# Kernel tuning notes

Hardware: AMD Instinct MI355X
Metric: run time of the kernel (lower is better)

The kernel has to match this reference:

```python
import jax, jax.numpy as jnp
import numpy as np

B = 16           # number of graphs
H = 8            # heads
NC = 9           # num_coeffs = (lmax+1)^2
DM = 128         # d_model (sphere_channels)
F = NC * DM      # flat_dim = 1152
HD = F // H      # head_dim = 144
RD = 16          # rope_dim
EPS = 1e-5


def setup_inputs() -> dict:
    key = jax.random.key(0)
    ks = jax.random.split(key, 8)
    N = 8192
    x_emb = jax.random.normal(ks[0], (N, NC, DM), dtype=jnp.float32)
    batch = jnp.sort(jax.random.randint(ks[1], (N,), 0, B)).astype(jnp.int32)
    pos = jax.random.normal(ks[2], (N, 3), dtype=jnp.float32) * 3.0
    Wqkv = jax.random.normal(ks[3], (F, 3 * F), dtype=jnp.float32) / np.sqrt(F)
    Wout = jax.random.normal(ks[4], (F, F), dtype=jnp.float32) / np.sqrt(F)
    rope_freqs = jax.random.normal(ks[5], (RD,), dtype=jnp.float32) * 0.1
    Wrope = jax.random.normal(ks[6], (RD, H), dtype=jnp.float32) / np.sqrt(RD)
    gamma = jnp.ones((F,), dtype=jnp.float32)
    beta = jnp.zeros((F,), dtype=jnp.float32)
    return {"x_emb": x_emb, "pos": pos, "Wqkv": Wqkv, "Wout": Wout,
            "rope_freqs": rope_freqs, "Wrope": Wrope,
            "gamma": gamma, "beta": beta, "batch": batch}


def _pad_layout(batch, N):
    # sorted batch ids -> per-node rank within its graph, sizes per graph
    sizes = jnp.bincount(batch, length=B)                       # [B]
    offsets = jnp.concatenate([jnp.zeros((1,), sizes.dtype), jnp.cumsum(sizes)[:-1]])
    rank = jnp.arange(N, dtype=sizes.dtype) - offsets[batch]    # [N]
    n_max = int(np.asarray(jax.device_get(sizes)).max())        # concrete pad width
    return sizes, rank, n_max


def reference(x_emb, pos, Wqkv, Wout, rope_freqs, Wrope, gamma, beta, batch):
    N = x_emb.shape[0]
    x_flat = x_emb.reshape(N, F)
    sizes, rank, n_max = _pad_layout(batch, N)

    # dense padding  [B, N_max, *]; mask True = padding slot
    x_pad = jnp.zeros((B, n_max, F), x_flat.dtype).at[batch, rank].set(x_flat)
    pos_pad = jnp.zeros((B, n_max, 3), pos.dtype).at[batch, rank].set(pos)
    mask = jnp.arange(n_max)[None, :] >= sizes[:, None]         # [B, N_max]

    qkv = x_pad @ Wqkv                                          # [B, N_max, 3F]
    q, k, v = jnp.split(qkv, 3, axis=-1)
    def heads(t):
        return t.reshape(B, n_max, H, HD).transpose(0, 2, 1, 3)  # [B,H,N_max,HD]
    q, k, v = heads(q), heads(k), heads(v)

    scale = HD ** (-0.5)
    attn = jnp.einsum('bhid,bhjd->bhij', q, k) * scale          # [B,H,N,N]

    # Fourier distance bias
    diff = pos_pad[:, :, None, :] - pos_pad[:, None, :, :]      # [B,N,N,3]
    dist = jnp.linalg.norm(diff, axis=-1)                       # [B,N,N]
    fourier = jnp.cos(dist[..., None] * jnp.abs(rope_freqs))    # [B,N,N,RD]
    bias = jnp.einsum('bijr,rh->bhij', fourier, Wrope)          # [B,H,N,N]
    pad_mask = mask[:, None, :] | mask[:, :, None]              # [B,N,N]
    bias = jnp.where(pad_mask[:, None, :, :], 0.0, bias)
    attn = attn + bias

    attn = jnp.where(mask[:, None, None, :], -jnp.inf, attn)    # key mask
    attn = jax.nn.softmax(attn, axis=-1)
    attn = jnp.nan_to_num(attn)

    out = jnp.einsum('bhij,bhjd->bhid', attn, v)                # [B,H,N,HD]
    out = out.transpose(0, 2, 1, 3).reshape(B, n_max, F) @ Wout
    out_flat = out[batch, rank]                                 # gather back [N,F]

    h = x_flat + out_flat
    mu = jnp.mean(h, axis=-1, keepdims=True)
    var = jnp.var(h, axis=-1, keepdims=True)
    y = (h - mu) / jnp.sqrt(var + EPS) * gamma + beta
    return y.reshape(N, NC, DM)
```

## Files before the change

kernel.cpp:

```cpp
#include <hip/hip_runtime.h>

typedef unsigned short u16;
typedef unsigned int   u32;
typedef __attribute__((ext_vector_type(8)))  __bf16 bf16x8;
typedef __attribute__((ext_vector_type(4)))  float  f32x4;
typedef __attribute__((ext_vector_type(16))) float  f32x16;
typedef __attribute__((ext_vector_type(4)))  u32    u32x4;
typedef __attribute__((ext_vector_type(2)))  u32    u32x2;

#define F_DIM   1152
#define QKV_DIM 3456
#define HD_SCALE 0.083333333333333333f
#define LOG2E    1.4426950408889634f
#define KSC      (HD_SCALE*LOG2E)
#define MAX4    80
#define BIAS_BLKS 2048

static __device__ __forceinline__ u16 f2bf(float f){
    u32 u = __builtin_bit_cast(u32, f);
    u32 r = u + 0x7fffu + ((u >> 16) & 1u);
    return (u16)(r >> 16);
}
static __device__ __forceinline__ u32 cvtpk(float lo, float hi){
    u32 r;
    asm("v_cvt_pk_bf16_f32 %0, %1, %2" : "=v"(r) : "v"(lo), "v"(hi));
    return r;
}

typedef __attribute__((address_space(1))) void gvoid;
typedef __attribute__((address_space(3))) void lvoid;
static __device__ __forceinline__ void gload16(const u16* g, u16* l){
    __builtin_amdgcn_global_load_lds((gvoid*)g, (lvoid*)l, 16, 0, 0);
}

__global__ __launch_bounds__(256) void prep_kernel(
        const float* __restrict__ x, u16* __restrict__ xb, int nCast, int n4,
        const float* __restrict__ Wqkv, u16* __restrict__ wqkvT,
        const float* __restrict__ Wout, u16* __restrict__ woutT,
        const float* __restrict__ pos, const float* __restrict__ rfreq,
        const float* __restrict__ Wrope, u16* __restrict__ biasP,
        const int* __restrict__ batch, int* __restrict__ meta, int N){
    __shared__ float tile[32][33];
    __shared__ int goffs[17];
    __shared__ int bpre[17];
    const int b = blockIdx.x, t = threadIdx.x;
    const int T1 = (QKV_DIM/32)*(F_DIM/32);
    const int T2 = (F_DIM/32)*(F_DIM/32);

    if (b < BIAS_BLKS){
        if (t <= 16){
            int lo = 0, hi = N;
            while (lo < hi){ int mid = (lo+hi)>>1; if (batch[mid] < t) lo = mid+1; else hi = mid; }
            goffs[t] = lo;
        }
        __syncthreads();
        if (t == 0){
            int bc = 0;
            for (int g = 0; g < 16; g++){
                bpre[g] = bc;
                int ng = goffs[g+1] - goffs[g];
                int ntg = (ng + 31) >> 5;
                bc += ntg*ntg;
            }
            bpre[16] = bc;
        }
        __syncthreads();
        float absf[16], w[16][8];
        #pragma unroll
        for (int r = 0; r < 16; r++){
            absf[r] = fabsf(rfreq[r]);
            #pragma unroll
            for (int h = 0; h < 8; h++) w[r][h] = Wrope[r*8 + h] * LOG2E;
        }
        const int total = bpre[16];
        for (int bb = b; bb < total; bb += BIAS_BLKS){
            int g = 0;
            while (bpre[g+1] <= bb) g++;
            int rem  = bb - bpre[g];
            int goff = goffs[g];
            int ng   = goffs[g+1] - goff;
            int ntg  = (ng + 31) >> 5;
            int qt   = rem / ntg;
            int jt   = rem - qt*ntg;
            size_t base = (size_t)bb * 8192;
            #pragma unroll
            for (int pp = 0; pp < 2; pp++){
                const int p0 = pp*512 + 2*t;
                float bv0[8], bv1[8];
                #pragma unroll
                for (int h = 0; h < 8; h++){ bv0[h] = 0.f; bv1[h] = 0.f; }
                const int i = p0 >> 5;
                int qn = goff + qt*32 + i;  if (qn >= goff + ng) qn = goff + ng - 1;
                float qx = pos[qn*3+0], qy = pos[qn*3+1], qz = pos[qn*3+2];
                #pragma unroll
                for (int e = 0; e < 2; e++){
                    int c = (p0 + e) & 31;
                    int p4 = c & 15;
                    int j  = (p4 & 3) + ((p4 >> 2) << 3) + ((c >> 4) << 2);
                    int kn = goff + jt*32 + j;  if (kn >= goff + ng) kn = goff + ng - 1;
                    float dx = qx - pos[kn*3+0];
                    float dy = qy - pos[kn*3+1];
                    float dz = qz - pos[kn*3+2];
                    float d  = sqrtf(dx*dx + dy*dy + dz*dz);
                    float* bv = e ? bv1 : bv0;
                    #pragma unroll
                    for (int r = 0; r < 16; r++){
                        float cs = __cosf(d * absf[r]);
                        #pragma unroll
                        for (int h = 0; h < 8; h++) bv[h] = fmaf(cs, w[r][h], bv[h]);
                    }
                }
                #pragma unroll
                for (int h = 0; h < 8; h++)
                    *(u32*)&biasP[base + h*1024 + p0] = cvtpk(bv0[h], bv1[h]);
            }
        }
        return;
    }
    const int b2 = b - BIAS_BLKS;
    if (b2 < nCast){
        int i = b2*256 + t;
        if (i < n4){
            float4 v = ((const float4*)x)[i];
            u32x2 o; o[0] = cvtpk(v.x, v.y); o[1] = cvtpk(v.z, v.w);
            *(u32x2*)&xb[(size_t)i*4] = o;
        }
        return;
    }
    if (b2 < nCast + T1 + T2){
        const float* in; u16* out; int R, C, bi;
        if (b2 < nCast + T1){ in = Wqkv; out = wqkvT; R = F_DIM; C = QKV_DIM; bi = b2 - nCast; }
        else                { in = Wout; out = woutT; R = F_DIM; C = F_DIM;  bi = b2 - nCast - T1; }
        int gx = C/32;
        int c0 = (bi % gx)*32, r0 = (bi / gx)*32;
        int tx = t & 31, ty = t >> 5;
        #pragma unroll
        for (int yy = ty; yy < 32; yy += 8)
            tile[yy][tx] = in[(size_t)(r0+yy)*C + (c0+tx)];
        __syncthreads();
        #pragma unroll
        for (int yy = ty; yy < 32; yy += 8)
            out[(size_t)(c0+yy)*R + (r0+tx)] = f2bf(tile[tx][yy]);
        return;
    }
    if (t <= 16){
        int lo = 0, hi = N;
        while (lo < hi){ int mid = (lo+hi)>>1; if (batch[mid] < t) lo = mid+1; else hi = mid; }
        meta[1+t] = lo;
    }
    __syncthreads();
    if (t == 0){
        int ps = 0, bcnt = 0, cnt4 = 0;
        for (int g = 0; g < 16; g++){
            int ng = meta[2+g] - meta[1+g];
            meta[20+g] = ps;
            meta[40+g] = bcnt;
            int nt = (ng + 31) / 32;
            ps += nt * 32;
            bcnt += nt * nt;
            int nt4 = (nt + 3) / 4;
            for (int q4 = 0; q4 < nt4; q4++){
                meta[64 + cnt4] = g;
                meta[64 + MAX4 + cnt4] = q4;
                cnt4++;
            }
        }
        meta[36] = ps;
        meta[56] = bcnt;
        meta[0]  = cnt4;
    }
}

template<bool OUT_BF16>
__global__ __launch_bounds__(512, 2) void gemm256(const u16* __restrict__ A,
                                                  const u16* __restrict__ Bt,
                                                  void* __restrict__ Cp,
                                                  int M, int Ncols, int K){
    __shared__ u16 sA[4][8192];
    __shared__ u16 sB[4][8192];
    const int nwg = gridDim.x;
    int orig = blockIdx.x;
    int qq = nwg >> 3, rr = nwg & 7;
    int xcd = orig & 7, pos = orig >> 3;
    int nid = (xcd < rr ? xcd*(qq+1) : rr*(qq+1) + (xcd-rr)*qq) + pos;
    const int gx = M >> 8;
    const int bm = (nid % gx) << 8, bn = (nid / gx) << 8;

    const int tid = threadIdx.x;
    const int w = tid >> 6, lane = tid & 63;
    const int wr = w >> 2, wc = w & 3;
    const int fr = lane & 15, fq = lane >> 4;
    const int swz8 = (fq ^ ((fr >> 1) & 3)) * 8;

    const u16* aS[2]; const u16* bS[2]; int dOf[2];
    #pragma unroll
    for (int p = 0; p < 2; p++){
        int idx = p*512 + tid;
        int row = idx >> 2, c = idx & 3;
        int sc = c ^ ((row >> 1) & 3);
        int brow = bn + row; if (brow > Ncols-1) brow = Ncols-1;
        aS[p] = A  + (size_t)(bm + row)*K + sc*8;
        bS[p] = Bt + (size_t)brow*K + sc*8;
        dOf[p] = idx*8;
    }

    f32x4 acc[8][4];
    #pragma unroll
    for (int m = 0; m < 8; m++)
        #pragma unroll
        for (int n = 0; n < 4; n++)
            #pragma unroll
            for (int e = 0; e < 4; e++) acc[m][n][e] = 0.f;

    const int nk = K >> 5;
    #pragma unroll
    for (int p = 0; p < 2; p++){ gload16(aS[p], &sA[0][dOf[p]]); gload16(bS[p], &sB[0][dOf[p]]); }
    #pragma unroll
    for (int p = 0; p < 2; p++){ gload16(aS[p]+32, &sA[1][dOf[p]]); gload16(bS[p]+32, &sB[1][dOf[p]]); }

    #pragma unroll 1
    for (int t = 0; t < nk; t++){
        int tp = (t+2 < nk) ? t+2 : nk-1;
        int bufS = (t+2) & 3;
        #pragma unroll
        for (int p = 0; p < 2; p++){
            gload16(aS[p] + tp*32, &sA[bufS][dOf[p]]);
            gload16(bS[p] + tp*32, &sB[bufS][dOf[p]]);
        }
        asm volatile("s_waitcnt vmcnt(8)\n\ts_barrier" ::: "memory");

        const u16* sAc = &sA[t & 3][0];
        const u16* sBc = &sB[t & 3][0];
        bf16x8 af[8], bfr[4];
        #pragma unroll
        for (int m = 0; m < 8; m++)
            af[m] = *(const bf16x8*)(sAc + (wr*128 + m*16 + fr)*32 + swz8);
        #pragma unroll
        for (int n = 0; n < 4; n++)
            bfr[n] = *(const bf16x8*)(sBc + (wc*64 + n*16 + fr)*32 + swz8);
        __builtin_amdgcn_s_setprio(1);
        #pragma unroll
        for (int m = 0; m < 8; m++)
            #pragma unroll
            for (int n = 0; n < 4; n++)
                acc[m][n] = __builtin_amdgcn_mfma_f32_16x16x32_bf16(af[m], bfr[n], acc[m][n], 0, 0, 0);
        __builtin_amdgcn_s_setprio(0);
    }

    #pragma unroll
    for (int m = 0; m < 8; m++)
        #pragma unroll
        for (int n = 0; n < 4; n++)
            #pragma unroll
            for (int r = 0; r < 4; r++){
                int row = bm + wr*128 + m*16 + fq*4 + r;
                int col = bn + wc*64 + n*16 + fr;
                if (col < Ncols){
                    float v = acc[m][n][r];
                    if (OUT_BF16) ((u16*)Cp)[(size_t)row*Ncols + col] = f2bf(v);
                    else          ((float*)Cp)[(size_t)row*Ncols + col] = v;
                }
            }
}

__global__ __launch_bounds__(256) void pack_v(const u16* __restrict__ qkv,
                                              u16* __restrict__ Vpack,
                                              const int* __restrict__ batch,
                                              const int* __restrict__ meta,
                                              int PT){
    __shared__ u16 tile[32][33];
    int nt0 = blockIdx.x*32, dt0 = blockIdx.y*32, h = blockIdx.z;
    int tx = threadIdx.x & 31, ty = threadIdx.x >> 5;
    #pragma unroll
    for (int yy = ty; yy < 32; yy += 8){
        int node = nt0+yy, d = dt0+tx;
        tile[yy][tx] = (d < 144) ? qkv[(size_t)node*QKV_DIM + 2*F_DIM + h*144 + d] : (u16)0;
    }
    __syncthreads();
    int node = nt0 + tx;
    int g = batch[node];
    int col = meta[20+g] + (node - meta[1+g]);
    int pt = col >> 5, cl = col & 31;
    #pragma unroll
    for (int yy = ty; yy < 32; yy += 8){
        int d = dt0+yy;
        if (d < 144) Vpack[(((size_t)h*PT + pt)*144 + d)*32 + cl] = tile[tx][yy];
    }
}

__global__ __launch_bounds__(256) void attn_kernel(
        const u16* __restrict__ qkv, const u16* __restrict__ Vpack,
        const u16* __restrict__ biasP, u16* __restrict__ attn_out,
        const int* __restrict__ meta, int PT){
    __shared__ u16 sK[2][4864];
    __shared__ u16 sV[2][4608];
    const int h = blockIdx.x & 7, t4 = blockIdx.x >> 3;
    if (t4 >= meta[0]) return;
    const int g    = meta[64 + t4];
    const int q4   = meta[64 + MAX4 + t4];
    const int goff = meta[1+g], gend = meta[2+g];
    const int ng   = gend - goff;
    const int ntg  = (ng + 31) >> 5;
    const int pst  = meta[20+g];
    const int boffg= meta[40+g];

    const int tid = threadIdx.x;
    const int w = tid >> 6, lane = tid & 63;
    const int li = lane & 31, hi = lane >> 5;
    const int qt = q4*4 + w;
    const int qbase = goff + qt*32;
    const int qtP = (qt < ntg) ? qt : (ntg - 1);

    int kOff[3];
    #pragma unroll
    for (int p = 0; p < 3; p++){
        int idx = p*256 + tid;
        if (idx > 607) idx = 607;
        int row = idx/19, c = idx - row*19;
        if (c == 18) c = 0;
        kOff[p] = row*QKV_DIM + c*8;
    }
    const u16* kBase = qkv + (size_t)goff*QKV_DIM + F_DIM + h*144;
    int vOff[3];
    #pragma unroll
    for (int p = 0; p < 3; p++){
        int idx = p*256 + tid;
        if (idx > 575) idx = 575;
        int d = idx >> 2, c = idx & 3;
        vOff[p] = d*32 + ((c ^ (d & 3)) << 3);
    }
    const u16* vBase = Vpack + ((size_t)h*PT + (pst >> 5))*4608;
    const u16* bBase = biasP + ((size_t)boffg + (size_t)qtP*ntg)*8192 + h*1024 + li*32 + hi*16;

    int qnode = qbase + li; if (qnode >= gend) qnode = gend - 1;
    const u16* qrow = qkv + (size_t)qnode*QKV_DIM + h*144;
    bf16x8 qf[9];
    #pragma unroll
    for (int kk = 0; kk < 9; kk++) qf[kk] = *(const bf16x8*)(qrow + kk*16 + hi*8);

    int jlr[16];
    #pragma unroll
    for (int r = 0; r < 16; r++) jlr[r] = (r & 3) + ((r >> 2) << 3) + (hi << 2);

    float lrun = 0.f;
    f32x16 O[5];
    #pragma unroll
    for (int dt = 0; dt < 5; dt++)
        #pragma unroll
        for (int e = 0; e < 16; e++) O[dt][e] = 0.f;

    u32x4 bA0, bA1, bN0, bN1;
    bA0 = *(const u32x4*)bBase;
    bA1 = *(const u32x4*)(bBase + 8);
    {
        gload16(kBase + kOff[0], &sK[0][tid*8]);
        gload16(kBase + kOff[1], &sK[0][(256+tid)*8]);
        if (tid < 96) gload16(kBase + kOff[2], &sK[0][(512+tid)*8]);
        gload16(vBase + vOff[0], &sV[0][tid*8]);
        gload16(vBase + vOff[1], &sV[0][(256+tid)*8]);
        if (tid < 64) gload16(vBase + vOff[2], &sV[0][(512+tid)*8]);
    }
    __syncthreads();

    #pragma unroll 1
    for (int t = 0; t < ntg; t++){
        const int cur = t & 1;
        int tn = (t+1 < ntg) ? t+1 : ntg-1;
        bN0 = *(const u32x4*)(bBase + (size_t)tn*8192);
        bN1 = *(const u32x4*)(bBase + (size_t)tn*8192 + 8);
        __builtin_amdgcn_sched_barrier(0);
        if (t+1 < ntg){
            const u16* kb = kBase + (size_t)(t+1)*32*QKV_DIM;
            const u16* vb = vBase + (size_t)(t+1)*4608;
            gload16(kb + kOff[0], &sK[cur^1][tid*8]);
            gload16(kb + kOff[1], &sK[cur^1][(256+tid)*8]);
            if (tid < 96) gload16(kb + kOff[2], &sK[cur^1][(512+tid)*8]);
            gload16(vb + vOff[0], &sV[cur^1][tid*8]);
            gload16(vb + vOff[1], &sV[cur^1][(256+tid)*8]);
            if (tid < 64) gload16(vb + vOff[2], &sV[cur^1][(512+tid)*8]);
        }

        const u16* sKc = &sK[cur][0];
        f32x16 sacc;
        #pragma unroll
        for (int e = 0; e < 16; e++) sacc[e] = 0.f;
        __builtin_amdgcn_s_setprio(1);
        #pragma unroll
        for (int kk = 0; kk < 9; kk++){
            bf16x8 kf = *(const bf16x8*)(sKc + li*152 + kk*16 + hi*8);
            sacc = __builtin_amdgcn_mfma_f32_32x32x16_bf16(kf, qf[kk], sacc, 0, 0, 0);
        }
        __builtin_amdgcn_s_setprio(0);

        float bfv[16];
        #pragma unroll
        for (int q = 0; q < 4; q++){
            bfv[2*q]     = __builtin_bit_cast(float, bA0[q] << 16);
            bfv[2*q+1]   = __builtin_bit_cast(float, bA0[q] & 0xffff0000u);
            bfv[8+2*q]   = __builtin_bit_cast(float, bA1[q] << 16);
            bfv[8+2*q+1] = __builtin_bit_cast(float, bA1[q] & 0xffff0000u);
        }

        const int j0 = t*32;
        float p[16];
        float psum = 0.f;
        if (j0 + 32 <= ng){
            #pragma unroll
            for (int r = 0; r < 16; r++){
                float s_ = fminf(fmaf(sacc[r], KSC, bfv[r]), 86.f);
                p[r] = exp2f(s_); psum += p[r];
            }
        } else {
            #pragma unroll
            for (int r = 0; r < 16; r++){
                float s_ = fminf(fmaf(sacc[r], KSC, bfv[r]), 86.f);
                p[r] = (j0 + jlr[r] < ng) ? exp2f(s_) : 0.f;
                psum += p[r];
            }
        }
        psum += __shfl_xor(psum, 32);
        lrun += psum;

        u32 cpk[8], opk[8];
        #pragma unroll
        for (int q = 0; q < 8; q++) cpk[q] = cvtpk(p[2*q], p[2*q+1]);
        #pragma unroll
        for (int q = 0; q < 8; q++) opk[q] = (u32)__shfl_xor((int)cpk[q], 32);
        u32x4 a0, a1;
        if (hi == 0){
            a0[0]=cpk[0]; a0[1]=cpk[1]; a0[2]=opk[0]; a0[3]=opk[1];
            a1[0]=cpk[4]; a1[1]=cpk[5]; a1[2]=opk[4]; a1[3]=opk[5];
        } else {
            a0[0]=opk[2]; a0[1]=opk[3]; a0[2]=cpk[2]; a0[3]=cpk[3];
            a1[0]=opk[6]; a1[1]=opk[7]; a1[2]=cpk[6]; a1[3]=cpk[7];
        }
        bf16x8 paf0 = __builtin_bit_cast(bf16x8, a0);
        bf16x8 paf1 = __builtin_bit_cast(bf16x8, a1);

        const u16* sVc = &sV[cur][0];
        __builtin_amdgcn_s_setprio(1);
        #pragma unroll
        for (int dt = 0; dt < 5; dt++){
            int d = dt*32 + li;
            int dc = (d > 143) ? 143 : d;
            int swzlo = ((hi     ^ (dc & 3)) << 3);
            int swzhi = (((2+hi) ^ (dc & 3)) << 3);
            bf16x8 v0 = *(const bf16x8*)(sVc + dc*32 + swzlo);
            bf16x8 v1 = *(const bf16x8*)(sVc + dc*32 + swzhi);
            O[dt] = __builtin_amdgcn_mfma_f32_32x32x16_bf16(paf0, v0, O[dt], 0, 0, 0);
            O[dt] = __builtin_amdgcn_mfma_f32_32x32x16_bf16(paf1, v1, O[dt], 0, 0, 0);
        }
        __builtin_amdgcn_s_setprio(0);

        bA0 = bN0; bA1 = bN1;
        __syncthreads();
    }

    if (qt < ntg){
        float lr[16];
        #pragma unroll
        for (int r = 0; r < 16; r++) lr[r] = 1.0f / __shfl(lrun, jlr[r]);
        #pragma unroll
        for (int dt = 0; dt < 5; dt++){
            int d = dt*32 + li;
            if (d < 144){
                #pragma unroll
                for (int r = 0; r < 16; r++){
                    int qi = jlr[r];
                    if (qt*32 + qi < ng)
                        attn_out[(size_t)(qbase + qi)*F_DIM + h*144 + d] = f2bf(O[dt][r]*lr[r]);
                }
            }
        }
    }
}

__global__ __launch_bounds__(256) void ln_kernel(const float* __restrict__ x,
                                                 float* __restrict__ io,
                                                 const float* __restrict__ gamma,
                                                 const float* __restrict__ beta){
    const int node = blockIdx.x;
    const float* xr = x  + (size_t)node*F_DIM;
    float* yr       = io + (size_t)node*F_DIM;
    const int t = threadIdx.x;
    float h[5]; float s = 0.f, ss = 0.f;
    #pragma unroll
    for (int i = 0; i < 5; i++){
        int idx = t + i*256;
        float v = 0.f;
        if (idx < F_DIM) v = xr[idx] + yr[idx];
        h[i] = v; s += v; ss += v*v;
    }
    #pragma unroll
    for (int o = 32; o > 0; o >>= 1){ s += __shfl_down(s, o); ss += __shfl_down(ss, o); }
    __shared__ float rs[4], rss[4];
    __shared__ float smu, srstd;
    if ((t & 63) == 0){ rs[t>>6] = s; rss[t>>6] = ss; }
    __syncthreads();
    if (t == 0){
        float S  = rs[0]+rs[1]+rs[2]+rs[3];
        float SS = rss[0]+rss[1]+rss[2]+rss[3];
        float mu = S * (1.f/F_DIM);
        float var = SS * (1.f/F_DIM) - mu*mu;
        smu = mu; srstd = rsqrtf(var + 1e-5f);
    }
    __syncthreads();
    float mu = smu, rstd = srstd;
    #pragma unroll
    for (int i = 0; i < 5; i++){
        int idx = t + i*256;
        if (idx < F_DIM) yr[idx] = (h[i]-mu)*rstd*gamma[idx] + beta[idx];
    }
}

extern "C" void kernel_launch(void* const* d_in, const int* in_sizes, int n_in,
                              void* d_out, int out_size, void* d_ws, size_t ws_size,
                              hipStream_t stream){
    const float* x     = (const float*)d_in[0];
    const float* pos   = (const float*)d_in[1];
    const float* Wqkv  = (const float*)d_in[2];
    const float* Wout  = (const float*)d_in[3];
    const float* rfreq = (const float*)d_in[4];
    const float* Wrope = (const float*)d_in[5];
    const float* gamma = (const float*)d_in[6];
    const float* beta  = (const float*)d_in[7];
    const int*   batch = (const int*)d_in[8];

    const int N  = in_sizes[0] / F_DIM;
    const int PN = N + 512;
    const int PT = PN / 32;

    char* ws = (char*)d_ws;
    size_t off = 0;
    auto alloc = [&](size_t b){ size_t o = off; off += (b + 255) & ~(size_t)255; return o; };
    int* meta   = (int*)(ws + alloc((size_t)(64 + 2*MAX4 + 64)*sizeof(int)));
    u16* xb     = (u16*)(ws + alloc((size_t)N*F_DIM*2));
    u16* wqkvT  = (u16*)(ws + alloc((size_t)QKV_DIM*F_DIM*2));
    u16* woutT  = (u16*)(ws + alloc((size_t)F_DIM*F_DIM*2));
    u16* qkv    = (u16*)(ws + alloc((size_t)N*QKV_DIM*2));
    u16* Vpack  = (u16*)(ws + alloc((size_t)8*PT*144*32*2));
    u16* biasb  = (u16*)(ws + off);
    (void)ws_size; (void)n_in; (void)out_size;

    const int n4    = N*F_DIM/4;
    const int nCast = (n4 + 255)/256;
    const int nT    = (QKV_DIM/32)*(F_DIM/32) + (F_DIM/32)*(F_DIM/32);
    hipLaunchKernelGGL(prep_kernel, dim3(BIAS_BLKS + nCast + nT + 1), dim3(256), 0, stream,
                       x, xb, nCast, n4, Wqkv, wqkvT, Wout, woutT,
                       pos, rfreq, Wrope, biasb, batch, meta, N);
    hipLaunchKernelGGL((gemm256<true>), dim3((N/256)*((QKV_DIM+255)/256)), dim3(512), 0, stream,
                       xb, wqkvT, (void*)qkv, N, QKV_DIM, F_DIM);
    hipLaunchKernelGGL(pack_v, dim3(N/32, 5, 8), dim3(256), 0, stream,
                       qkv, Vpack, batch, meta, PT);
    hipLaunchKernelGGL(attn_kernel, dim3(MAX4*8), dim3(256), 0, stream,
                       qkv, Vpack, biasb, xb, meta, PT);
    hipLaunchKernelGGL((gemm256<false>), dim3((N/256)*((F_DIM+255)/256)), dim3(512), 0, stream,
                       xb, woutT, d_out, N, F_DIM, F_DIM);
    hipLaunchKernelGGL(ln_kernel, dim3(N), dim3(256), 0, stream,
                       x, (float*)d_out, gamma, beta);
}
```

Measured before the change: 287.3 us.

## Interleave bias compute and memory-bound prep work within persistent prep blocks

```diff
diff --git a/kernel.cpp b/kernel.cpp
--- a/kernel.cpp
+++ b/kernel.cpp
@@ -14,7 +14,7 @@
 #define LOG2E    1.4426950408889634f
 #define KSC      (HD_SCALE*LOG2E)
 #define MAX4    80
-#define BIAS_BLKS 2048
+#define PREP_BLKS 4096
 
 static __device__ __forceinline__ u16 f2bf(float f){
     u32 u = __builtin_bit_cast(u32, f);
@@ -46,25 +46,27 @@
     const int b = blockIdx.x, t = threadIdx.x;
     const int T1 = (QKV_DIM/32)*(F_DIM/32);
     const int T2 = (F_DIM/32)*(F_DIM/32);
-
-    if (b < BIAS_BLKS){
-        if (t <= 16){
-            int lo = 0, hi = N;
-            while (lo < hi){ int mid = (lo+hi)>>1; if (batch[mid] < t) lo = mid+1; else hi = mid; }
-            goffs[t] = lo;
-        }
-        __syncthreads();
-        if (t == 0){
-            int bc = 0;
-            for (int g = 0; g < 16; g++){
-                bpre[g] = bc;
-                int ng = goffs[g+1] - goffs[g];
-                int ntg = (ng + 31) >> 5;
-                bc += ntg*ntg;
-            }
-            bpre[16] = bc;
-        }
-        __syncthreads();
+    const int NMEM = nCast + T1 + T2 + 1;
+
+    if (t <= 16){
+        int lo = 0, hi = N;
+        while (lo < hi){ int mid = (lo+hi)>>1; if (batch[mid] < t) lo = mid+1; else hi = mid; }
+        goffs[t] = lo;
+    }
+    __syncthreads();
+    if (t == 0){
+        int bc = 0;
+        for (int g = 0; g < 16; g++){
+            bpre[g] = bc;
+            int ng = goffs[g+1] - goffs[g];
+            int ntg = (ng + 31) >> 5;
+            bc += ntg*ntg;
+        }
+        bpre[16] = bc;
+    }
+    __syncthreads();
+
+    auto do_bias = [&](){
         float absf[16], w[16][8];
         #pragma unroll
         for (int r = 0; r < 16; r++){
@@ -73,7 +75,7 @@
             for (int h = 0; h < 8; h++) w[r][h] = Wrope[r*8 + h] * LOG2E;
         }
         const int total = bpre[16];
-        for (int bb = b; bb < total; bb += BIAS_BLKS){
+        for (int bb = b; bb < total; bb += PREP_BLKS){
             int g = 0;
             while (bpre[g+1] <= bb) g++;
             int rem  = bb - bpre[g];
@@ -115,60 +117,61 @@
                     *(u32*)&biasP[base + h*1024 + p0] = cvtpk(bv0[h], bv1[h]);
             }
         }
-        return;
-    }
-    const int b2 = b - BIAS_BLKS;
-    if (b2 < nCast){
-        int i = b2*256 + t;
-        if (i < n4){
-            float4 v = ((const float4*)x)[i];
-            u32x2 o; o[0] = cvtpk(v.x, v.y); o[1] = cvtpk(v.z, v.w);
-            *(u32x2*)&xb[(size_t)i*4] = o;
-        }
-        return;
-    }
-    if (b2 < nCast + T1 + T2){
-        const float* in; u16* out; int R, C, bi;
-        if (b2 < nCast + T1){ in = Wqkv; out = wqkvT; R = F_DIM; C = QKV_DIM; bi = b2 - nCast; }
-        else                { in = Wout; out = woutT; R = F_DIM; C = F_DIM;  bi = b2 - nCast - T1; }
-        int gx = C/32;
-        int c0 = (bi % gx)*32, r0 = (bi / gx)*32;
-        int tx = t & 31, ty = t >> 5;
-        #pragma unroll
-        for (int yy = ty; yy < 32; yy += 8)
-            tile[yy][tx] = in[(size_t)(r0+yy)*C + (c0+tx)];
-        __syncthreads();
-        #pragma unroll
-        for (int yy = ty; yy < 32; yy += 8)
-            out[(size_t)(c0+yy)*R + (r0+tx)] = f2bf(tile[tx][yy]);
-        return;
-    }
-    if (t <= 16){
-        int lo = 0, hi = N;
-        while (lo < hi){ int mid = (lo+hi)>>1; if (batch[mid] < t) lo = mid+1; else hi = mid; }
-        meta[1+t] = lo;
-    }
-    __syncthreads();
-    if (t == 0){
-        int ps = 0, bcnt = 0, cnt4 = 0;
-        for (int g = 0; g < 16; g++){
-            int ng = meta[2+g] - meta[1+g];
-            meta[20+g] = ps;
-            meta[40+g] = bcnt;
-            int nt = (ng + 31) / 32;
-            ps += nt * 32;
-            bcnt += nt * nt;
-            int nt4 = (nt + 3) / 4;
-            for (int q4 = 0; q4 < nt4; q4++){
-                meta[64 + cnt4] = g;
-                meta[64 + MAX4 + cnt4] = q4;
-                cnt4++;
+    };
+
+    auto do_mem = [&](){
+        for (int u = b; u < NMEM; u += PREP_BLKS){
+            if (u < nCast){
+                int i = u*256 + t;
+                if (i < n4){
+                    float4 v = ((const float4*)x)[i];
+                    u32x2 o; o[0] = cvtpk(v.x, v.y); o[1] = cvtpk(v.z, v.w);
+                    *(u32x2*)&xb[(size_t)i*4] = o;
+                }
+            } else if (u < nCast + T1 + T2){
+                const float* in; u16* out; int R, C, bi;
+                if (u < nCast + T1){ in = Wqkv; out = wqkvT; R = F_DIM; C = QKV_DIM; bi = u - nCast; }
+                else               { in = Wout; out = woutT; R = F_DIM; C = F_DIM;  bi = u - nCast - T1; }
+                int gx = C/32;
+                int c0 = (bi % gx)*32, r0 = (bi / gx)*32;
+                int tx = t & 31, ty = t >> 5;
+                __syncthreads();
+                #pragma unroll
+                for (int yy = ty; yy < 32; yy += 8)
+                    tile[yy][tx] = in[(size_t)(r0+yy)*C + (c0+tx)];
+                __syncthreads();
+                #pragma unroll
+                for (int yy = ty; yy < 32; yy += 8)
+                    out[(size_t)(c0+yy)*R + (r0+tx)] = f2bf(tile[tx][yy]);
+            } else {
+                if (t <= 16) meta[1+t] = goffs[t];
+                __syncthreads();
+                if (t == 0){
+                    int ps = 0, bcnt = 0, cnt4 = 0;
+                    for (int g = 0; g < 16; g++){
+                        int ng = meta[2+g] - meta[1+g];
+                        meta[20+g] = ps;
+                        meta[40+g] = bcnt;
+                        int nt = (ng + 31) / 32;
+                        ps += nt * 32;
+                        bcnt += nt * nt;
+                        int nt4 = (nt + 3) / 4;
+                        for (int q4 = 0; q4 < nt4; q4++){
+                            meta[64 + cnt4] = g;
+                            meta[64 + MAX4 + cnt4] = q4;
+                            cnt4++;
+                        }
+                    }
+                    meta[36] = ps;
+                    meta[56] = bcnt;
+                    meta[0]  = cnt4;
+                }
             }
         }
-        meta[36] = ps;
-        meta[56] = bcnt;
-        meta[0]  = cnt4;
-    }
+    };
+
+    if (b & 1){ do_bias(); do_mem(); }
+    else      { do_mem(); do_bias(); }
 }
 
 template<bool OUT_BF16>
@@ -544,8 +547,7 @@
 
     const int n4    = N*F_DIM/4;
     const int nCast = (n4 + 255)/256;
-    const int nT    = (QKV_DIM/32)*(F_DIM/32) + (F_DIM/32)*(F_DIM/32);
-    hipLaunchKernelGGL(prep_kernel, dim3(BIAS_BLKS + nCast + nT + 1), dim3(256), 0, stream,
+    hipLaunchKernelGGL(prep_kernel, dim3(PREP_BLKS), dim3(256), 0, stream,
                        x, xb, nCast, n4, Wqkv, wqkvT, Wout, woutT,
                        pos, rfreq, Wrope, biasb, batch, meta, N);
     hipLaunchKernelGGL((gemm256<true>), dim3((N/256)*((QKV_DIM+255)/256)), dim3(512), 0, stream,
```

Measured after the change: 291.5 us. Within noise of the previous version (+1.5%).
